# Optimization experiments

Measured on AMD Instinct MI355X. Metric: run time of the kernel, lower is better.

Reference implementation:

```python
import jax, jax.numpy as jnp
import numpy as np

N_NODES = 50000
N_EDGES = 600000
IN_FEATS = 128
OUT_FEATS = 128


def setup_inputs() -> dict:
    key = jax.random.key(0)
    k1, k2, k3, k4, k5 = jax.random.split(key, 5)
    feature = jax.random.normal(k1, (N_NODES, IN_FEATS), dtype=jnp.float32)
    src = jax.random.randint(k2, (N_EDGES,), 0, N_NODES, dtype=jnp.int64)
    dst = jax.random.randint(k3, (N_EDGES,), 0, N_NODES, dtype=jnp.int64)
    # nn.Linear params (PyTorch stores weight as [out, in])
    bound = 1.0 / np.sqrt(IN_FEATS)
    W = jax.random.uniform(k4, (OUT_FEATS, IN_FEATS), dtype=jnp.float32, minval=-bound, maxval=bound)
    b = jax.random.uniform(k5, (OUT_FEATS,), dtype=jnp.float32, minval=-bound, maxval=bound)
    return {"feature": feature, "W": W, "b": b, "src": src, "dst": dst}


def reference(feature, W, b, src, dst):
    # copy_src + sum: aggregate src features onto dst nodes (SpMM)
    agg = jax.ops.segment_sum(feature[src], dst, num_segments=N_NODES)  # [N, in]
    # linear + tanh
    return jnp.tanh(agg @ W.T + b)  # [N, out]
```

## Files before the change

### kernel.cpp

```cpp
#include <hip/hip_runtime.h>
#include <hip/hip_fp16.h>
#include <math.h>

constexpr int kNodes = 50000;
constexpr int kEdges = 600000;
constexpr int kF     = 128;
constexpr int kNPB   = 64;
constexpr int kCap   = 48;
constexpr int kCurStride = 16;
constexpr int kEPT   = 4;

constexpr int kGemmB = (kNodes + kNPB - 1) / kNPB;
constexpr int kFillB = (kEdges + 256 * kEPT - 1) / (256 * kEPT);

constexpr size_t kOffWt     = 0;
constexpr size_t kOffCursor = 65536;
constexpr size_t kOffBucket = kOffCursor + (size_t)kNodes * kCurStride * 4;
constexpr size_t kOffGpk    = kOffBucket + (size_t)kNodes * kCap * 2;
constexpr size_t kWsNeeded  = kOffGpk + (size_t)kNodes * kF * 2;

typedef _Float16 f16x8 __attribute__((ext_vector_type(8)));
typedef float    f32x4 __attribute__((ext_vector_type(4)));

static __device__ __forceinline__ unsigned int packh2(float a, float b) {
    __half2 h = __floats2half2_rn(a, b);
    return *reinterpret_cast<unsigned int*>(&h);
}

__global__ __launch_bounds__(256) void prep0(const float* __restrict__ W,
                                             _Float16* __restrict__ Wf,
                                             int* __restrict__ cursor) {
    int gid = blockIdx.x * 256 + threadIdx.x;
    if (gid < kF * kF) {
        int e  = gid & 7;
        int l  = (gid >> 3) & 63;
        int ks = (gid >> 9) & 3;
        int nt = gid >> 11;
        int o  = nt * 16 + (l & 15);
        int k  = ks * 32 + ((l >> 4) & 3) * 8 + e;
        Wf[gid] = (_Float16)W[o * kF + k];
    }
    if (gid < kNodes) cursor[gid * kCurStride] = 0;
}

__global__ __launch_bounds__(256) void prep0_fb(const float* __restrict__ W,
                                                float* __restrict__ Wt,
                                                int* __restrict__ cursor) {
    int gid = blockIdx.x * 256 + threadIdx.x;
    if (gid < kF * kF) {
        int k = gid >> 7;
        int o = gid & (kF - 1);
        Wt[gid] = W[o * kF + k];
    }
    if (gid < kNodes) cursor[gid * kCurStride] = 0;
}

__global__ __launch_bounds__(256) void fill(const int* __restrict__ src,
                                            const int* __restrict__ dst,
                                            int* __restrict__ cursor,
                                            unsigned short* __restrict__ bucket) {
    const int gid = blockIdx.x * 256 + threadIdx.x;
    const int e0  = gid * kEPT;
    if (e0 + kEPT <= kEdges) {
        int4 d4 = *reinterpret_cast<const int4*>(dst + e0);
        int4 s4 = *reinterpret_cast<const int4*>(src + e0);
        int dd[4] = {d4.x, d4.y, d4.z, d4.w};
        int ss[4] = {s4.x, s4.y, s4.z, s4.w};
#pragma unroll
        for (int i = 0; i < kEPT; ++i) {
            int p = atomicAdd(&cursor[(size_t)dd[i] * kCurStride], 1);
            if (p < kCap) bucket[(size_t)dd[i] * kCap + p] = (unsigned short)ss[i];
        }
    } else if (e0 < kEdges) {
        for (int e = e0; e < kEdges; ++e) {
            int d = dst[e];
            int p = atomicAdd(&cursor[(size_t)d * kCurStride], 1);
            if (p < kCap) bucket[(size_t)d * kCap + p] = (unsigned short)src[e];
        }
    }
}

__global__ __launch_bounds__(256) void gemm(const float* __restrict__ F,
                                            const _Float16* __restrict__ Wf,
                                            uint2* __restrict__ Gpk2) {
    const int t = threadIdx.x;
    const int b = blockIdx.x;

    const int n0  = b * kNPB;
    const int w   = t >> 6;
    const int l   = t & 63;
    const int m0w = n0 + w * 16;
    if (m0w >= kNodes) return;
    const int node  = m0w + (l & 15);
    const int nodeC = node < kNodes ? node : kNodes - 1;
    const int kbase = (l >> 4) * 8;

    f32x4 acc[8];
#pragma unroll
    for (int nt = 0; nt < 8; ++nt) acc[nt] = (f32x4){0.f, 0.f, 0.f, 0.f};

    const f16x8* Wf8 = reinterpret_cast<const f16x8*>(Wf);

#pragma unroll
    for (int ks = 0; ks < 4; ++ks) {
        const float* fr = F + (size_t)nodeC * kF + ks * 32 + kbase;
        float4 x = *reinterpret_cast<const float4*>(fr);
        float4 y = *reinterpret_cast<const float4*>(fr + 4);
        float fv[8] = {x.x, x.y, x.z, x.w, y.x, y.y, y.z, y.w};
        f16x8 bhi, blo;
#pragma unroll
        for (int i = 0; i < 8; ++i) {
            _Float16 h = (_Float16)fv[i];
            bhi[i] = h;
            blo[i] = (_Float16)(fv[i] - (float)h);
        }
#pragma unroll
        for (int nt = 0; nt < 8; ++nt) {
            f16x8 af = Wf8[(nt * 4 + ks) * 64 + l];
            acc[nt] = __builtin_amdgcn_mfma_f32_16x16x32_f16(af, bhi, acc[nt], 0, 0, 0);
            acc[nt] = __builtin_amdgcn_mfma_f32_16x16x32_f16(af, blo, acc[nt], 0, 0, 0);
        }
    }

    if (node < kNodes) {
#pragma unroll
        for (int nt = 0; nt < 8; ++nt) {
            uint2 p;
            p.x = packh2(acc[nt][0], acc[nt][1]);
            p.y = packh2(acc[nt][2], acc[nt][3]);
            Gpk2[(size_t)node * 32 + nt * 4 + (l >> 4)] = p;
        }
    }
}

__global__ __launch_bounds__(256) void gather_tanh(const uint4* __restrict__ Gpk4,
                                                   const unsigned short* __restrict__ bucket,
                                                   const int* __restrict__ cursor,
                                                   const float* __restrict__ bias,
                                                   float* __restrict__ out) {
    const int wave = (blockIdx.x * 256 + threadIdx.x) >> 6;
    const int lane = threadIdx.x & 63;
    if (wave >= kNodes) return;
    const int grp = lane >> 4;
    const int sub = lane & 15;

    const int deg = min(cursor[(size_t)wave * kCurStride], kCap);
    const size_t base = (size_t)wave * kCap;

    int eid = (lane < deg) ? (int)bucket[base + lane] : 0;

    float acc[8];
#pragma unroll
    for (int i = 0; i < 8; ++i) acc[i] = 0.0f;

    const int iters = (deg + 3) >> 2;
#pragma unroll 2
    for (int i = 0; i < iters; ++i) {
        const int j = grp + 4 * i;
        const bool valid = (j < deg);
        int s = __shfl(eid, valid ? j : 0);
        if (valid) {
            uint4 u = Gpk4[(size_t)s * 16 + sub];
            const __half2* hp = reinterpret_cast<const __half2*>(&u);
#pragma unroll
            for (int q = 0; q < 4; ++q) {
                float2 f = __half22float2(hp[q]);
                acc[2 * q]     += f.x;
                acc[2 * q + 1] += f.y;
            }
        }
    }

#pragma unroll
    for (int i = 0; i < 8; ++i) {
        acc[i] += __shfl_xor(acc[i], 16);
        acc[i] += __shfl_xor(acc[i], 32);
    }

    if (grp == 0) {
        float4 b0 = *reinterpret_cast<const float4*>(bias + sub * 8);
        float4 b1 = *reinterpret_cast<const float4*>(bias + sub * 8 + 4);
        float4 r0, r1;
        r0.x = 1.0f - 2.0f / (__expf(2.0f * (acc[0] + b0.x)) + 1.0f);
        r0.y = 1.0f - 2.0f / (__expf(2.0f * (acc[1] + b0.y)) + 1.0f);
        r0.z = 1.0f - 2.0f / (__expf(2.0f * (acc[2] + b0.z)) + 1.0f);
        r0.w = 1.0f - 2.0f / (__expf(2.0f * (acc[3] + b0.w)) + 1.0f);
        r1.x = 1.0f - 2.0f / (__expf(2.0f * (acc[4] + b1.x)) + 1.0f);
        r1.y = 1.0f - 2.0f / (__expf(2.0f * (acc[5] + b1.y)) + 1.0f);
        r1.z = 1.0f - 2.0f / (__expf(2.0f * (acc[6] + b1.z)) + 1.0f);
        r1.w = 1.0f - 2.0f / (__expf(2.0f * (acc[7] + b1.w)) + 1.0f);
        float4* dstp = reinterpret_cast<float4*>(out + (size_t)wave * kF + sub * 8);
        dstp[0] = r0;
        dstp[1] = r1;
    }
}

__global__ __launch_bounds__(256) void scatter_add(const float* __restrict__ feature,
                                                   const int* __restrict__ src,
                                                   const int* __restrict__ dst,
                                                   float* __restrict__ agg) {
    int gid = blockIdx.x * 256 + threadIdx.x;
    int e = gid >> 5;
    int c = (gid & 31) << 2;
    float4 v = *reinterpret_cast<const float4*>(feature + (size_t)src[e] * kF + c);
    float* p = agg + (size_t)dst[e] * kF + c;
    atomicAdd(p + 0, v.x);
    atomicAdd(p + 1, v.y);
    atomicAdd(p + 2, v.z);
    atomicAdd(p + 3, v.w);
}

__global__ __launch_bounds__(256, 4) void linear_tanh(float* __restrict__ inout,
                                                      const float* __restrict__ Wt,
                                                      const float* __restrict__ bias) {
    __shared__ float sAgg[kNPB * kF];
    __shared__ float sB[kF];
    const int t  = threadIdx.x;
    const int n0 = blockIdx.x * kNPB;
    if (t < kF) sB[t] = bias[t];
    const int rows = min(kNPB, kNodes - n0);
    for (int i = t * 4; i < rows * kF; i += 256 * 4)
        *reinterpret_cast<float4*>(&sAgg[i]) =
            *reinterpret_cast<const float4*>(inout + (size_t)n0 * kF + i);
    __syncthreads();
    const int tn = t >> 5, to = t & 31, nb = tn * 8;
    float acc[8][4];
#pragma unroll
    for (int n = 0; n < 8; ++n)
#pragma unroll
        for (int j = 0; j < 4; ++j) acc[n][j] = 0.0f;
    for (int k = 0; k < kF; k += 4) {
        float4 wt[4];
#pragma unroll
        for (int i = 0; i < 4; ++i)
            wt[i] = *reinterpret_cast<const float4*>(Wt + (k + i) * kF + to * 4);
#pragma unroll
        for (int n = 0; n < 8; ++n) {
            float4 av = *reinterpret_cast<const float4*>(&sAgg[(nb + n) * kF + k]);
#pragma unroll
            for (int j = 0; j < 4; ++j) {
                const float* w0 = reinterpret_cast<const float*>(&wt[0]);
                const float* w1 = reinterpret_cast<const float*>(&wt[1]);
                const float* w2 = reinterpret_cast<const float*>(&wt[2]);
                const float* w3 = reinterpret_cast<const float*>(&wt[3]);
                acc[n][j] += av.x * w0[j] + av.y * w1[j] + av.z * w2[j] + av.w * w3[j];
            }
        }
    }
#pragma unroll
    for (int n = 0; n < 8; ++n) {
        int node = n0 + nb + n;
        if (node < kNodes) {
            float4 r;
            r.x = 1.0f - 2.0f / (__expf(2.0f * (acc[n][0] + sB[to * 4 + 0])) + 1.0f);
            r.y = 1.0f - 2.0f / (__expf(2.0f * (acc[n][1] + sB[to * 4 + 1])) + 1.0f);
            r.z = 1.0f - 2.0f / (__expf(2.0f * (acc[n][2] + sB[to * 4 + 2])) + 1.0f);
            r.w = 1.0f - 2.0f / (__expf(2.0f * (acc[n][3] + sB[to * 4 + 3])) + 1.0f);
            *reinterpret_cast<float4*>(inout + (size_t)node * kF + to * 4) = r;
        }
    }
}

extern "C" void kernel_launch(void* const* d_in, const int* in_sizes, int n_in,
                              void* d_out, int out_size, void* d_ws, size_t ws_size,
                              hipStream_t stream) {
    const float* feature = (const float*)d_in[0];
    const float* W       = (const float*)d_in[1];
    const float* b       = (const float*)d_in[2];
    const int*   src     = (const int*)d_in[3];
    const int*   dst     = (const int*)d_in[4];
    float* out = (float*)d_out;

    char* ws = (char*)d_ws;
    _Float16* Wfrag  = (_Float16*)(ws + kOffWt);
    float*    Wt     = (float*)(ws + kOffWt);
    int*      cursor = (int*)(ws + kOffCursor);
    unsigned short* bucket = (unsigned short*)(ws + kOffBucket);
    uint2*    Gpk2   = (uint2*)(ws + kOffGpk);

    if (ws_size >= kWsNeeded) {
        prep0<<<(kNodes + 255) / 256, 256, 0, stream>>>(W, Wfrag, cursor);
        fill<<<kFillB, 256, 0, stream>>>(src, dst, cursor, bucket);
        gemm<<<kGemmB, 256, 0, stream>>>(feature, Wfrag, Gpk2);
        gather_tanh<<<(kNodes + 3) / 4, 256, 0, stream>>>(
            (const uint4*)Gpk2, bucket, cursor, b, out);
    } else {
        prep0_fb<<<(kNodes + 255) / 256, 256, 0, stream>>>(W, Wt, cursor);
        hipMemsetAsync(out, 0, (size_t)kNodes * kF * sizeof(float), stream);
        scatter_add<<<(kEdges * 32) / 256, 256, 0, stream>>>(feature, src, dst, out);
        linear_tanh<<<(kNodes + kNPB - 1) / kNPB, 256, 0, stream>>>(out, Wt, b);
    }
}
```

Before: 160.2 us.

## Merge edge bucketing and feature GEMM into one launch with prefetched loads

Combines the edge-bucket fill kernel and the per-node GEMM kernel into a single grid, where trailing blocks do the atomic bucket fill and leading blocks do the MFMA GEMM. This removes one launch and lets the latency-bound atomic work overlap with the compute-bound GEMM. The GEMM now loads all feature values up front and double-buffers the weight fragments, and adds a launch-bounds occupancy hint of 3. These changes raise register pressure, and the tail path for a partial final edge chunk is simplified to assume the edge count is divisible by four.

```diff
diff --git a/kernel.cpp b/kernel.cpp
--- a/kernel.cpp
+++ b/kernel.cpp
@@ -12,6 +12,7 @@
 
 constexpr int kGemmB = (kNodes + kNPB - 1) / kNPB;
 constexpr int kFillB = (kEdges + 256 * kEPT - 1) / (256 * kEPT);
+constexpr int kTotB  = kGemmB + kFillB;
 
 constexpr size_t kOffWt     = 0;
 constexpr size_t kOffCursor = 65536;
@@ -55,36 +56,32 @@
     if (gid < kNodes) cursor[gid * kCurStride] = 0;
 }
 
-__global__ __launch_bounds__(256) void fill(const int* __restrict__ src,
-                                            const int* __restrict__ dst,
-                                            int* __restrict__ cursor,
-                                            unsigned short* __restrict__ bucket) {
-    const int gid = blockIdx.x * 256 + threadIdx.x;
-    const int e0  = gid * kEPT;
-    if (e0 + kEPT <= kEdges) {
-        int4 d4 = *reinterpret_cast<const int4*>(dst + e0);
-        int4 s4 = *reinterpret_cast<const int4*>(src + e0);
-        int dd[4] = {d4.x, d4.y, d4.z, d4.w};
-        int ss[4] = {s4.x, s4.y, s4.z, s4.w};
-#pragma unroll
-        for (int i = 0; i < kEPT; ++i) {
-            int p = atomicAdd(&cursor[(size_t)dd[i] * kCurStride], 1);
-            if (p < kCap) bucket[(size_t)dd[i] * kCap + p] = (unsigned short)ss[i];
-        }
-    } else if (e0 < kEdges) {
-        for (int e = e0; e < kEdges; ++e) {
-            int d = dst[e];
-            int p = atomicAdd(&cursor[(size_t)d * kCurStride], 1);
-            if (p < kCap) bucket[(size_t)d * kCap + p] = (unsigned short)src[e];
-        }
-    }
-}
-
-__global__ __launch_bounds__(256) void gemm(const float* __restrict__ F,
-                                            const _Float16* __restrict__ Wf,
-                                            uint2* __restrict__ Gpk2) {
+__global__ __launch_bounds__(256, 3) void gemm_fill(const float* __restrict__ F,
+                                                    const _Float16* __restrict__ Wf,
+                                                    const int* __restrict__ src,
+                                                    const int* __restrict__ dst,
+                                                    int* __restrict__ cursor,
+                                                    unsigned short* __restrict__ bucket,
+                                                    uint2* __restrict__ Gpk2) {
     const int t = threadIdx.x;
     const int b = blockIdx.x;
+
+    if (b >= kGemmB) {
+        const int gid = (b - kGemmB) * 256 + t;
+        const int e0  = gid * kEPT;
+        if (e0 < kEdges) {
+            int4 d4 = *reinterpret_cast<const int4*>(dst + e0);
+            int4 s4 = *reinterpret_cast<const int4*>(src + e0);
+            int dd[4] = {d4.x, d4.y, d4.z, d4.w};
+            int ss[4] = {s4.x, s4.y, s4.z, s4.w};
+#pragma unroll
+            for (int i = 0; i < kEPT; ++i) {
+                int p = atomicAdd(&cursor[(size_t)dd[i] * kCurStride], 1);
+                if (p < kCap) bucket[(size_t)dd[i] * kCap + p] = (unsigned short)ss[i];
+            }
+        }
+        return;
+    }
 
     const int n0  = b * kNPB;
     const int w   = t >> 6;
@@ -95,30 +92,52 @@
     const int nodeC = node < kNodes ? node : kNodes - 1;
     const int kbase = (l >> 4) * 8;
 
+    const f16x8* Wf8 = reinterpret_cast<const f16x8*>(Wf);
+    const float* frow = F + (size_t)nodeC * kF + kbase;
+
+    float4 f4[8];
+#pragma unroll
+    for (int ks = 0; ks < 4; ++ks) {
+        f4[ks * 2 + 0] = *reinterpret_cast<const float4*>(frow + ks * 32);
+        f4[ks * 2 + 1] = *reinterpret_cast<const float4*>(frow + ks * 32 + 4);
+    }
+
+    f16x8 wq[8];
+#pragma unroll
+    for (int nt = 0; nt < 8; ++nt) wq[nt] = Wf8[(nt * 4 + 0) * 64 + l];
+
+    f16x8 bhi[4], blo[4];
+#pragma unroll
+    for (int ks = 0; ks < 4; ++ks) {
+        const float* fv0 = reinterpret_cast<const float*>(&f4[ks * 2]);
+#pragma unroll
+        for (int i = 0; i < 8; ++i) {
+            float v = fv0[i];
+            _Float16 h = (_Float16)v;
+            bhi[ks][i] = h;
+            blo[ks][i] = (_Float16)(v - (float)h);
+        }
+    }
+
     f32x4 acc[8];
 #pragma unroll
     for (int nt = 0; nt < 8; ++nt) acc[nt] = (f32x4){0.f, 0.f, 0.f, 0.f};
 
-    const f16x8* Wf8 = reinterpret_cast<const f16x8*>(Wf);
-
 #pragma unroll
     for (int ks = 0; ks < 4; ++ks) {
-        const float* fr = F + (size_t)nodeC * kF + ks * 32 + kbase;
-        float4 x = *reinterpret_cast<const float4*>(fr);
-        float4 y = *reinterpret_cast<const float4*>(fr + 4);
-        float fv[8] = {x.x, x.y, x.z, x.w, y.x, y.y, y.z, y.w};
-        f16x8 bhi, blo;
-#pragma unroll
-        for (int i = 0; i < 8; ++i) {
-            _Float16 h = (_Float16)fv[i];
-            bhi[i] = h;
-            blo[i] = (_Float16)(fv[i] - (float)h);
+        f16x8 wn[8];
+        if (ks < 3) {
+#pragma unroll
+            for (int nt = 0; nt < 8; ++nt) wn[nt] = Wf8[(nt * 4 + ks + 1) * 64 + l];
         }
 #pragma unroll
         for (int nt = 0; nt < 8; ++nt) {
-            f16x8 af = Wf8[(nt * 4 + ks) * 64 + l];
-            acc[nt] = __builtin_amdgcn_mfma_f32_16x16x32_f16(af, bhi, acc[nt], 0, 0, 0);
-            acc[nt] = __builtin_amdgcn_mfma_f32_16x16x32_f16(af, blo, acc[nt], 0, 0, 0);
+            acc[nt] = __builtin_amdgcn_mfma_f32_16x16x32_f16(wq[nt], bhi[ks], acc[nt], 0, 0, 0);
+            acc[nt] = __builtin_amdgcn_mfma_f32_16x16x32_f16(wq[nt], blo[ks], acc[nt], 0, 0, 0);
+        }
+        if (ks < 3) {
+#pragma unroll
+            for (int nt = 0; nt < 8; ++nt) wq[nt] = wn[nt];
         }
     }
 
@@ -280,8 +299,8 @@
 
     if (ws_size >= kWsNeeded) {
         prep0<<<(kNodes + 255) / 256, 256, 0, stream>>>(W, Wfrag, cursor);
-        fill<<<kFillB, 256, 0, stream>>>(src, dst, cursor, bucket);
-        gemm<<<kGemmB, 256, 0, stream>>>(feature, Wfrag, Gpk2);
+        gemm_fill<<<kTotB, 256, 0, stream>>>(
+            feature, Wfrag, src, dst, cursor, bucket, Gpk2);
         gather_tanh<<<(kNodes + 3) / 4, 256, 0, stream>>>(
             (const uint4*)Gpk2, bucket, cursor, b, out);
     } else {
```

New measurement: 143.8 us. 10.3% less time.
